# Kernel tuning notes

Measured on AMD Instinct MI355X. Metric: run time of the kernel, lower is better.

Reference implementation:

```python
import jax, jax.numpy as jnp
import numpy as np

EPS_POOL = 1e-9
NEG_INF = -1e9
TEMPERATURE = 0.07


def _l2norm(x, axis=-1, eps=1e-12):
    # matches torch F.normalize(p=2): x / max(||x||, eps)
    n = jnp.sqrt(jnp.sum(x * x, axis=axis, keepdims=True))
    return x / jnp.maximum(n, eps)


def setup_inputs() -> dict:
    key = jax.random.key(0)
    ks = jax.random.split(key, 8)
    B, Lq, Lc, D = 256, 128, 512, 384
    question_tokens = jax.random.normal(ks[0], (B, Lq, D), dtype=jnp.float32)
    chunk_tokens = jax.random.normal(ks[1], (B, Lc, D), dtype=jnp.float32)
    q_mask = jax.random.randint(ks[2], (B, Lq), 0, 2, dtype=jnp.int32)
    c_mask = jax.random.randint(ks[3], (B, Lc), 0, 2, dtype=jnp.int32)
    # ensure at least one valid token per row (avoid fully-masked rows)
    q_mask = q_mask.at[:, 0].set(1)
    c_mask = c_mask.at[:, 0].set(1)
    W1 = jax.random.normal(ks[4], (D, D), dtype=jnp.float32) * (1.0 / np.sqrt(D))
    b1 = jnp.zeros((D,), dtype=jnp.float32)
    W2 = jax.random.normal(ks[5], (D, D), dtype=jnp.float32) * (1.0 / np.sqrt(D))
    b2 = jnp.zeros((D,), dtype=jnp.float32)
    return {"question_tokens": question_tokens, "chunk_tokens": chunk_tokens,
            "q_mask": q_mask, "c_mask": c_mask,
            "W1": W1, "b1": b1, "W2": W2, "b2": b2}


def _encode(tokens, mask, W1, b1, W2, b2):
    # mean pool over valid tokens: [B,L,D] -> [B,D]
    m = mask.astype(tokens.dtype)[..., None]
    pooled = jnp.sum(tokens * m, axis=1) / jnp.maximum(jnp.sum(m, axis=1), EPS_POOL)
    h = jax.nn.relu(pooled @ W1 + b1)
    proj = h @ W2 + b2
    return _l2norm(proj, axis=1)


def _late_interaction(q_tokens, c_tokens, q_mask, c_mask):
    qn = _l2norm(q_tokens)                      # [B,Lq,D]
    cn = _l2norm(c_tokens)                      # [B,Lc,D]
    sims = jnp.einsum('bqd,bkd->bqk', qn, cn)   # [B,Lq,Lc]
    valid = q_mask[:, :, None].astype(bool) & c_mask[:, None, :].astype(bool)
    sims = jnp.where(valid, sims, NEG_INF)
    max_sim = jnp.max(sims, axis=-1)            # [B,Lq]
    max_sim = jnp.where(q_mask.astype(bool), max_sim, 0.0)
    return jnp.sum(max_sim, axis=-1)            # [B]


def reference(question_tokens, chunk_tokens, q_mask, c_mask, W1, b1, W2, b2):
    q_emb = _encode(question_tokens, q_mask, W1, b1, W2, b2)  # [B,D]
    c_emb = _encode(chunk_tokens, c_mask, W1, b1, W2, b2)     # [B,D]
    contrastive_sim = (q_emb @ c_emb.T) / TEMPERATURE         # [B,B]
    late_sim = _late_interaction(question_tokens, chunk_tokens, q_mask, c_mask)  # [B]
    return contrastive_sim, late_sim
```

## Files before the change

### kernel.cpp

```cpp
#include <hip/hip_runtime.h>
#include <hip/hip_bf16.h>
#include <stdint.h>

#define NB 256
#define LQ 128
#define LC 512
#define DIM 384
#define TCD 32
#define QP 392

typedef __attribute__((ext_vector_type(8))) short short8;
typedef __attribute__((ext_vector_type(4))) float f32x4;

__device__ __forceinline__ unsigned short f2bf(float x) {
  union { float f; uint32_t u; } c; c.f = x;
  return (unsigned short)((c.u + 0x7fffu + ((c.u >> 16) & 1u)) >> 16);
}

__global__ __launch_bounds__(512, 1)
void fused_pool_late(const float* __restrict__ qtok, const float* __restrict__ ctok,
                     const int* __restrict__ qm, const int* __restrict__ cm,
                     float* __restrict__ pooled, float* __restrict__ late) {
  __shared__ unsigned short s_q[LQ][QP];
  __shared__ unsigned short s_c[TCD][QP];
  __shared__ float s_pq[8][DIM];
  __shared__ float s_pc[8][DIM];
  __shared__ float s_cnt[2][8];
  __shared__ int   s_cval[TCD];
  __shared__ float s_wsum[8];

  const int b = blockIdx.x;
  const int tid = threadIdx.x;
  const int wave = tid >> 6;
  const int lane = tid & 63;
  const int rA = lane & 15;
  const int kof = (lane >> 4) * 8;

  const float* qb = qtok + (size_t)b * LQ * DIM;
  const float* cb = ctok + (size_t)b * LC * DIM;
  const int* qmb = qm + b * LQ;
  const int* cmb = cm + b * LC;

  float pq[6] = {0.f,0.f,0.f,0.f,0.f,0.f};
  float cq = 0.f;
  for (int r0 = 0; r0 < 16; ++r0) {
    const int r = wave * 16 + r0;
    const float* src = qb + r * DIM;
    float v[6], ss = 0.f;
#pragma unroll
    for (int j = 0; j < 6; ++j) { v[j] = src[lane + 64 * j]; ss += v[j] * v[j]; }
#pragma unroll
    for (int o = 32; o; o >>= 1) ss += __shfl_xor(ss, o);
    const float inv = 1.0f / fmaxf(sqrtf(ss), 1e-12f);
    const float fm = (float)qmb[r];
#pragma unroll
    for (int j = 0; j < 6; ++j) {
      s_q[r][lane + 64 * j] = f2bf(v[j] * inv);
      pq[j] = fmaf(v[j], fm, pq[j]);
    }
    cq += fm;
  }
#pragma unroll
  for (int j = 0; j < 6; ++j) s_pq[wave][lane + 64 * j] = pq[j];
  if (lane == 0) s_cnt[0][wave] = cq;

  float rm[4] = {-1e9f, -1e9f, -1e9f, -1e9f};
  float pc[6] = {0.f,0.f,0.f,0.f,0.f,0.f};
  float cc = 0.f;

  for (int t = 0; t < LC / TCD; ++t) {
    __syncthreads();
#pragma unroll
    for (int r0 = 0; r0 < 4; ++r0) {
      const int r = wave * 4 + r0;
      const int crow = t * TCD + r;
      const float* src = cb + crow * DIM;
      float v[6], ss = 0.f;
#pragma unroll
      for (int j = 0; j < 6; ++j) { v[j] = src[lane + 64 * j]; ss += v[j] * v[j]; }
#pragma unroll
      for (int o = 32; o; o >>= 1) ss += __shfl_xor(ss, o);
      const float inv = 1.0f / fmaxf(sqrtf(ss), 1e-12f);
      const int mk = cmb[crow];
      const float fm = (float)mk;
#pragma unroll
      for (int j = 0; j < 6; ++j) {
        s_c[r][lane + 64 * j] = f2bf(v[j] * inv);
        pc[j] = fmaf(v[j], fm, pc[j]);
      }
      cc += fm;
      if (lane == 0) s_cval[r] = mk;
    }
    __syncthreads();

    const unsigned short* ap  = &s_q[wave * 16 + rA][kof];
    const unsigned short* bp0 = &s_c[rA][kof];
    const unsigned short* bp1 = &s_c[rA + 16][kof];
    f32x4 acc0 = {0.f,0.f,0.f,0.f};
    f32x4 acc1 = {0.f,0.f,0.f,0.f};
#pragma unroll
    for (int kk = 0; kk < 12; ++kk) {
      short8 a  = *(const short8*)(ap  + kk * 32);
      short8 b0 = *(const short8*)(bp0 + kk * 32);
      short8 b1 = *(const short8*)(bp1 + kk * 32);
      acc0 = __builtin_amdgcn_mfma_f32_16x16x32_bf16(a, b0, acc0, 0, 0, 0);
      acc1 = __builtin_amdgcn_mfma_f32_16x16x32_bf16(a, b1, acc1, 0, 0, 0);
    }
    const bool v0 = s_cval[rA] != 0;
    const bool v1 = s_cval[rA + 16] != 0;
#pragma unroll
    for (int r = 0; r < 4; ++r) {
      const float a0 = v0 ? acc0[r] : -1e9f;
      const float a1 = v1 ? acc1[r] : -1e9f;
      rm[r] = fmaxf(rm[r], fmaxf(a0, a1));
    }
  }

#pragma unroll
  for (int j = 0; j < 6; ++j) s_pc[wave][lane + 64 * j] = pc[j];
  if (lane == 0) s_cnt[1][wave] = cc;

#pragma unroll
  for (int r = 0; r < 4; ++r) {
#pragma unroll
    for (int o = 1; o < 16; o <<= 1) rm[r] = fmaxf(rm[r], __shfl_xor(rm[r], o));
  }
  float ps = 0.f;
  if (rA == 0) {
    const int rowb = wave * 16 + (lane >> 4) * 4;
#pragma unroll
    for (int r = 0; r < 4; ++r) ps += qmb[rowb + r] ? rm[r] : 0.f;
  }
#pragma unroll
  for (int o = 32; o; o >>= 1) ps += __shfl_xor(ps, o);
  if (lane == 0) s_wsum[wave] = ps;
  __syncthreads();

  if (tid < DIM) {
    float sq = 0.f, sc = 0.f, nq = 0.f, nc = 0.f;
#pragma unroll
    for (int w = 0; w < 8; ++w) {
      sq += s_pq[w][tid];
      sc += s_pc[w][tid];
      nq += s_cnt[0][w];
      nc += s_cnt[1][w];
    }
    pooled[b * DIM + tid] = sq / fmaxf(nq, 1e-9f);
    pooled[(NB + b) * DIM + tid] = sc / fmaxf(nc, 1e-9f);
  }
  if (tid == 0) {
    float tot = 0.f;
#pragma unroll
    for (int w = 0; w < 8; ++w) tot += s_wsum[w];
    late[b] = tot;
  }
}

__global__ __launch_bounds__(DIM)
void mlp_kernel(const float* __restrict__ pooled,
                const float* __restrict__ W1, const float* __restrict__ b1,
                const float* __restrict__ W2, const float* __restrict__ b2,
                float* __restrict__ emb) {
  __shared__ float s_in[DIM];
  __shared__ float s_h[DIM];
  __shared__ float s_red[6];
  const int row = blockIdx.y * NB + blockIdx.x;
  const int d = threadIdx.x;
  s_in[d] = pooled[row * DIM + d];
  __syncthreads();
  float acc = b1[d];
#pragma unroll 8
  for (int k = 0; k < DIM; ++k) acc = fmaf(s_in[k], W1[k * DIM + d], acc);
  s_h[d] = fmaxf(acc, 0.f);
  __syncthreads();
  float p = b2[d];
#pragma unroll 8
  for (int k = 0; k < DIM; ++k) p = fmaf(s_h[k], W2[k * DIM + d], p);
  float ss = p * p;
#pragma unroll
  for (int o = 32; o; o >>= 1) ss += __shfl_xor(ss, o);
  if ((d & 63) == 0) s_red[d >> 6] = ss;
  __syncthreads();
  float tot = 0.f;
#pragma unroll
  for (int w = 0; w < 6; ++w) tot += s_red[w];
  emb[row * DIM + d] = p * (1.0f / fmaxf(sqrtf(tot), 1e-12f));
}

__global__ __launch_bounds__(NB)
void contrast_kernel(const float* __restrict__ emb, float* __restrict__ out0) {
  __shared__ float s_q[DIM];
  const int i = blockIdx.x;
  for (int k = threadIdx.x; k < DIM; k += NB) s_q[k] = emb[i * DIM + k];
  __syncthreads();
  const float* ce = emb + (size_t)(NB + threadIdx.x) * DIM;
  float acc = 0.f;
#pragma unroll 8
  for (int k = 0; k < DIM; ++k) acc = fmaf(s_q[k], ce[k], acc);
  out0[i * NB + threadIdx.x] = acc / 0.07f;
}

extern "C" void kernel_launch(void* const* d_in, const int* in_sizes, int n_in,
                              void* d_out, int out_size, void* d_ws, size_t ws_size,
                              hipStream_t stream) {
  const float* qtok = (const float*)d_in[0];
  const float* ctok = (const float*)d_in[1];
  const int*   qmm  = (const int*)d_in[2];
  const int*   cmm  = (const int*)d_in[3];
  const float* W1   = (const float*)d_in[4];
  const float* b1   = (const float*)d_in[5];
  const float* W2   = (const float*)d_in[6];
  const float* b2   = (const float*)d_in[7];

  float* out0 = (float*)d_out;
  float* late = out0 + NB * NB;
  float* pooled = (float*)d_ws;
  float* emb    = pooled + 2 * NB * DIM;

  hipLaunchKernelGGL(fused_pool_late, dim3(NB), dim3(512), 0, stream,
                     qtok, ctok, qmm, cmm, pooled, late);
  hipLaunchKernelGGL(mlp_kernel, dim3(NB, 2), dim3(DIM), 0, stream,
                     pooled, W1, b1, W2, b2, emb);
  hipLaunchKernelGGL(contrast_kernel, dim3(NB), dim3(NB), 0, stream, emb, out0);
}
```

Measured before the change: 134.7 us.

## Split fused pool/late kernel into normalize, pipelined maxsim, and merged MLP stages

Replaces the single 256-block fused kernel with a wide normalize+pool pass that writes bf16 normalized tokens to workspace. A separate maxsim kernel then reads them through a triple-buffered global_load_lds pipeline with swizzled LDS and register-held A fragments. A merge kernel runs the q and c MLPs together, sharing weight loads. The goal is more parallelism across CUs and overlap of loads with MFMA, at the cost of an extra bf16 round trip through HBM and a large workspace requirement. The old path is kept as a fallback when the workspace is too small.

```diff
diff --git a/kernel.cpp b/kernel.cpp
--- a/kernel.cpp
+++ b/kernel.cpp
@@ -6,21 +6,296 @@
 #define LQ 128
 #define LC 512
 #define DIM 384
+
+typedef __attribute__((ext_vector_type(8))) short short8;
+typedef __attribute__((ext_vector_type(4))) float f4;
+typedef __attribute__((ext_vector_type(2))) unsigned int u32x2;
+
+__device__ __forceinline__ unsigned int pk2bf(float a, float b) {
+  union { float f; uint32_t u; } x, y; x.f = a; y.f = b;
+  uint32_t lo = (x.u + 0x7fffu + ((x.u >> 16) & 1u)) >> 16;
+  uint32_t hi = (y.u + 0x7fffu + ((y.u >> 16) & 1u)) >> 16;
+  return lo | (hi << 16);
+}
+
+__device__ __forceinline__ void gload16(const void* g, void* l) {
+  __builtin_amdgcn_global_load_lds(
+      (const __attribute__((address_space(1))) void*)g,
+      (__attribute__((address_space(3))) void*)l, 16, 0, 0);
+}
+
+__device__ __forceinline__ void barrier_pinned() {
+  __builtin_amdgcn_sched_barrier(0);
+  __builtin_amdgcn_s_barrier();
+  __builtin_amdgcn_sched_barrier(0);
+}
+
+__device__ __forceinline__ void proc_row(const float* __restrict__ src, int mk,
+                                         unsigned short* __restrict__ dst, int lane,
+                                         f4& p0, f4& p1, float& cnt) {
+  const f4* p = (const f4*)src;
+  const f4 va = p[lane];
+  const f4 vb = p[64 + (lane & 31)];
+  float ss = va.x*va.x + va.y*va.y + va.z*va.z + va.w*va.w;
+  if (lane < 32) ss += vb.x*vb.x + vb.y*vb.y + vb.z*vb.z + vb.w*vb.w;
+#pragma unroll
+  for (int o = 32; o; o >>= 1) ss += __shfl_xor(ss, o);
+  const float inv = 1.0f / fmaxf(sqrtf(ss), 1e-12f);
+  const float fm = (float)mk;
+  p0 += va * fm;
+  if (lane < 32) p1 += vb * fm;
+  cnt += fm;
+  u32x2 w0; w0[0] = pk2bf(va.x * inv, va.y * inv); w0[1] = pk2bf(va.z * inv, va.w * inv);
+  *(u32x2*)(dst + 4 * lane) = w0;
+  if (lane < 32) {
+    u32x2 w1; w1[0] = pk2bf(vb.x * inv, vb.y * inv); w1[1] = pk2bf(vb.z * inv, vb.w * inv);
+    *(u32x2*)(dst + 256 + 4 * lane) = w1;
+  }
+}
+
+__global__ __launch_bounds__(256, 8)
+void normalize_pool(const float* __restrict__ qtok, const float* __restrict__ ctok,
+                    const int* __restrict__ qm, const int* __restrict__ cm,
+                    unsigned short* __restrict__ qn, unsigned short* __restrict__ cn,
+                    float* __restrict__ pp, float* __restrict__ nn) {
+  __shared__ float s_red[4][2][DIM];
+  __shared__ float s_cnt[4][2];
+  const int bid = blockIdx.x;
+  const int b = bid >> 3, s = bid & 7;
+  const int tid = threadIdx.x, wave = tid >> 6, lane = tid & 63;
+
+  f4 pq0 = {0,0,0,0}, pq1 = {0,0,0,0}, pc0 = {0,0,0,0}, pc1 = {0,0,0,0};
+  float cq = 0.f, cc = 0.f;
+
+#pragma unroll
+  for (int i = 0; i < 4; ++i) {
+    const int row = b * LQ + s * 16 + wave * 4 + i;
+    proc_row(qtok + (size_t)row * DIM, qm[row], qn + (size_t)row * DIM, lane, pq0, pq1, cq);
+  }
+#pragma unroll 4
+  for (int i = 0; i < 16; ++i) {
+    const int row = b * LC + s * 64 + wave * 16 + i;
+    proc_row(ctok + (size_t)row * DIM, cm[row], cn + (size_t)row * DIM, lane, pc0, pc1, cc);
+  }
+
+  *(f4*)&s_red[wave][0][4 * lane] = pq0;
+  if (lane < 32) *(f4*)&s_red[wave][0][256 + 4 * lane] = pq1;
+  *(f4*)&s_red[wave][1][4 * lane] = pc0;
+  if (lane < 32) *(f4*)&s_red[wave][1][256 + 4 * lane] = pc1;
+  if (lane == 0) { s_cnt[wave][0] = cq; s_cnt[wave][1] = cc; }
+  __syncthreads();
+
+  for (int d = tid; d < DIM; d += 256) {
+    float sq = 0.f, sc = 0.f;
+#pragma unroll
+    for (int w = 0; w < 4; ++w) { sq += s_red[w][0][d]; sc += s_red[w][1][d]; }
+    pp[(size_t)bid * 768 + d] = sq;
+    pp[(size_t)bid * 768 + DIM + d] = sc;
+  }
+  if (tid == 0) {
+    nn[bid * 2]     = s_cnt[0][0] + s_cnt[1][0] + s_cnt[2][0] + s_cnt[3][0];
+    nn[bid * 2 + 1] = s_cnt[0][1] + s_cnt[1][1] + s_cnt[2][1] + s_cnt[3][1];
+  }
+}
+
+__global__ __launch_bounds__(512, 4)
+void maxsim(const unsigned short* __restrict__ qn, const unsigned short* __restrict__ cn,
+            const int* __restrict__ cm, float* __restrict__ ws_rm) {
+  __shared__ __attribute__((aligned(128))) char ring[3][24576];
+  __shared__ int s_cm[256];
+  const int bid = blockIdx.x;
+  const int b = bid >> 1, s = bid & 1;
+  const int tid = threadIdx.x, wave = tid >> 6, lane = tid & 63;
+  const int rA = lane & 15, hi = lane >> 4;
+
+  if (tid < 256) s_cm[tid] = cm[b * LC + s * 256 + tid];
+  __syncthreads();
+
+  const char* qbase = (const char*)(qn + (size_t)b * LQ * DIM);
+  const char* cbase = (const char*)(cn + (size_t)b * LC * DIM) + (size_t)s * 256 * 768;
+
+  int goff[3];
+#pragma unroll
+  for (int j = 0; j < 3; ++j) {
+    const unsigned n = (unsigned)j * 512u + (unsigned)wave * 64u + (unsigned)lane;
+    const unsigned row = n / 48u, col = n % 48u;
+    goff[j] = (int)(row * 768u + ((col ^ (row & 7u)) << 4));
+  }
+
+#pragma unroll
+  for (int tile = 0; tile < 3; ++tile) {
+    char* dst = ring[tile] + wave * 1024;
+#pragma unroll
+    for (int j = 0; j < 3; ++j) gload16(qbase + tile * 24576 + goff[j], dst + j * 8192);
+  }
+  asm volatile("s_waitcnt vmcnt(0)" ::: "memory");
+  barrier_pinned();
+
+  short8 A[12] = {};
+  if (wave < 6) {
+    const char* bp = ring[wave >> 1];
+    const int lr = (wave & 1) * 16 + rA;
+#pragma unroll
+    for (int kk = 0; kk < 12; ++kk)
+      A[kk] = *(const short8*)(bp + lr * 768 + (((kk * 4 + hi) ^ (lr & 7)) << 4));
+    asm volatile("s_waitcnt lgkmcnt(0)" ::: "memory");
+  }
+  barrier_pinned();
+
+  {
+    char* dst = ring[0] + wave * 1024;
+#pragma unroll
+    for (int j = 0; j < 3; ++j) gload16(qbase + 3 * 24576 + goff[j], dst + j * 8192);
+  }
+  asm volatile("s_waitcnt vmcnt(0)" ::: "memory");
+  barrier_pinned();
+  if (wave >= 6) {
+    const char* bp = ring[0];
+    const int lr = (wave - 6) * 16 + rA;
+#pragma unroll
+    for (int kk = 0; kk < 12; ++kk)
+      A[kk] = *(const short8*)(bp + lr * 768 + (((kk * 4 + hi) ^ (lr & 7)) << 4));
+    asm volatile("s_waitcnt lgkmcnt(0)" ::: "memory");
+  }
+  barrier_pinned();
+
+#pragma unroll
+  for (int t0 = 0; t0 < 2; ++t0) {
+    char* dst = ring[t0 + 1] + wave * 1024;
+#pragma unroll
+    for (int j = 0; j < 3; ++j) gload16(cbase + (size_t)t0 * 24576 + goff[j], dst + j * 8192);
+  }
+
+  float rm[4] = {-1e9f, -1e9f, -1e9f, -1e9f};
+
+#pragma unroll
+  for (int t = 0; t < 8; ++t) {
+    if (t == 7) { asm volatile("s_waitcnt vmcnt(0)" ::: "memory"); }
+    else        { asm volatile("s_waitcnt vmcnt(3)" ::: "memory"); }
+    barrier_pinned();
+
+    const char* bp = ring[(t + 1) % 3];
+    f4 acc0 = {0,0,0,0}, acc1 = {0,0,0,0};
+#pragma unroll
+    for (int kk = 0; kk < 12; ++kk) {
+      const int sw = ((kk * 4 + hi) ^ (rA & 7)) << 4;
+      const short8 b0 = *(const short8*)(bp + rA * 768 + sw);
+      const short8 b1 = *(const short8*)(bp + (rA + 16) * 768 + sw);
+      acc0 = __builtin_amdgcn_mfma_f32_16x16x32_bf16(A[kk], b0, acc0, 0, 0, 0);
+      acc1 = __builtin_amdgcn_mfma_f32_16x16x32_bf16(A[kk], b1, acc1, 0, 0, 0);
+    }
+    if (t + 2 < 8) {
+      char* dst = ring[(t + 3) % 3] + wave * 1024;
+#pragma unroll
+      for (int j = 0; j < 3; ++j) gload16(cbase + (size_t)(t + 2) * 24576 + goff[j], dst + j * 8192);
+    }
+    const bool v0 = s_cm[t * 32 + rA] != 0;
+    const bool v1 = s_cm[t * 32 + rA + 16] != 0;
+#pragma unroll
+    for (int r = 0; r < 4; ++r) {
+      const float a0 = v0 ? acc0[r] : -1e9f;
+      const float a1 = v1 ? acc1[r] : -1e9f;
+      rm[r] = fmaxf(rm[r], fmaxf(a0, a1));
+    }
+  }
+
+#pragma unroll
+  for (int r = 0; r < 4; ++r) {
+#pragma unroll
+    for (int o = 1; o < 16; o <<= 1) rm[r] = fmaxf(rm[r], __shfl_xor(rm[r], o));
+  }
+  if (rA == 0) {
+#pragma unroll
+    for (int r = 0; r < 4; ++r)
+      ws_rm[(size_t)bid * LQ + wave * 16 + hi * 4 + r] = rm[r];
+  }
+}
+
+__global__ __launch_bounds__(DIM)
+void merge_mlp(const float* __restrict__ ws_rm, const float* __restrict__ pp,
+               const float* __restrict__ nn, const int* __restrict__ qm,
+               const float* __restrict__ W1, const float* __restrict__ b1,
+               const float* __restrict__ W2, const float* __restrict__ b2,
+               float* __restrict__ late, float* __restrict__ emb) {
+  __shared__ float s_q[DIM], s_c[DIM], s_hq[DIM], s_hc[DIM];
+  __shared__ float s_red[2][6], s_l[2];
+  const int b = blockIdx.x;
+  const int d = threadIdx.x;
+
+  if (d < LQ) {
+    const float m = fmaxf(ws_rm[(size_t)(2 * b) * LQ + d],
+                          ws_rm[(size_t)(2 * b + 1) * LQ + d]);
+    float ps = qm[b * LQ + d] ? m : 0.f;
+#pragma unroll
+    for (int o = 32; o; o >>= 1) ps += __shfl_xor(ps, o);
+    if ((d & 63) == 0) s_l[d >> 6] = ps;
+  }
+  float sq = 0.f, sc = 0.f, nq = 0.f, nc = 0.f;
+#pragma unroll
+  for (int s = 0; s < 8; ++s) {
+    sq += pp[(size_t)(b * 8 + s) * 768 + d];
+    sc += pp[(size_t)(b * 8 + s) * 768 + DIM + d];
+    nq += nn[(b * 8 + s) * 2];
+    nc += nn[(b * 8 + s) * 2 + 1];
+  }
+  s_q[d] = sq / fmaxf(nq, 1e-9f);
+  s_c[d] = sc / fmaxf(nc, 1e-9f);
+  __syncthreads();
+
+  float aq = b1[d], ac = b1[d];
+#pragma unroll 8
+  for (int k = 0; k < DIM; ++k) {
+    const float w = W1[k * DIM + d];
+    aq = fmaf(s_q[k], w, aq);
+    ac = fmaf(s_c[k], w, ac);
+  }
+  s_hq[d] = fmaxf(aq, 0.f);
+  s_hc[d] = fmaxf(ac, 0.f);
+  __syncthreads();
+  float pq = b2[d], pc = b2[d];
+#pragma unroll 8
+  for (int k = 0; k < DIM; ++k) {
+    const float w = W2[k * DIM + d];
+    pq = fmaf(s_hq[k], w, pq);
+    pc = fmaf(s_hc[k], w, pc);
+  }
+  float q2 = pq * pq, c2 = pc * pc;
+#pragma unroll
+  for (int o = 32; o; o >>= 1) { q2 += __shfl_xor(q2, o); c2 += __shfl_xor(c2, o); }
+  if ((d & 63) == 0) { s_red[0][d >> 6] = q2; s_red[1][d >> 6] = c2; }
+  __syncthreads();
+  float tq = 0.f, tc = 0.f;
+#pragma unroll
+  for (int w = 0; w < 6; ++w) { tq += s_red[0][w]; tc += s_red[1][w]; }
+  emb[(size_t)b * DIM + d] = pq * (1.0f / fmaxf(sqrtf(tq), 1e-12f));
+  emb[(size_t)(NB + b) * DIM + d] = pc * (1.0f / fmaxf(sqrtf(tc), 1e-12f));
+  if (d == 0) late[b] = s_l[0] + s_l[1];
+}
+
+__global__ __launch_bounds__(NB)
+void contrast_kernel(const float* __restrict__ emb, float* __restrict__ out0) {
+  __shared__ float s_q[DIM];
+  const int i = blockIdx.x;
+  for (int k = threadIdx.x; k < DIM; k += NB) s_q[k] = emb[(size_t)i * DIM + k];
+  __syncthreads();
+  const float* ce = emb + (size_t)(NB + threadIdx.x) * DIM;
+  float acc = 0.f;
+#pragma unroll 8
+  for (int k = 0; k < DIM; ++k) acc = fmaf(s_q[k], ce[k], acc);
+  out0[(size_t)i * NB + threadIdx.x] = acc / 0.07f;
+}
+
 #define TCD 32
 #define QP 392
-
-typedef __attribute__((ext_vector_type(8))) short short8;
-typedef __attribute__((ext_vector_type(4))) float f32x4;
-
 __device__ __forceinline__ unsigned short f2bf(float x) {
   union { float f; uint32_t u; } c; c.f = x;
   return (unsigned short)((c.u + 0x7fffu + ((c.u >> 16) & 1u)) >> 16);
 }
 
 __global__ __launch_bounds__(512, 1)
-void fused_pool_late(const float* __restrict__ qtok, const float* __restrict__ ctok,
-                     const int* __restrict__ qm, const int* __restrict__ cm,
-                     float* __restrict__ pooled, float* __restrict__ late) {
+void fused_v1(const float* __restrict__ qtok, const float* __restrict__ ctok,
+              const int* __restrict__ qm, const int* __restrict__ cm,
+              float* __restrict__ pooled, float* __restrict__ late) {
   __shared__ unsigned short s_q[LQ][QP];
   __shared__ unsigned short s_c[TCD][QP];
   __shared__ float s_pq[8][DIM];
@@ -96,8 +371,8 @@
     const unsigned short* ap  = &s_q[wave * 16 + rA][kof];
     const unsigned short* bp0 = &s_c[rA][kof];
     const unsigned short* bp1 = &s_c[rA + 16][kof];
-    f32x4 acc0 = {0.f,0.f,0.f,0.f};
-    f32x4 acc1 = {0.f,0.f,0.f,0.f};
+    f4 acc0 = {0.f,0.f,0.f,0.f};
+    f4 acc1 = {0.f,0.f,0.f,0.f};
 #pragma unroll
     for (int kk = 0; kk < 12; ++kk) {
       short8 a  = *(const short8*)(ap  + kk * 32);
@@ -157,16 +432,16 @@
 }
 
 __global__ __launch_bounds__(DIM)
-void mlp_kernel(const float* __restrict__ pooled,
-                const float* __restrict__ W1, const float* __restrict__ b1,
-                const float* __restrict__ W2, const float* __restrict__ b2,
-                float* __restrict__ emb) {
+void mlp_v1(const float* __restrict__ pooled,
+            const float* __restrict__ W1, const float* __restrict__ b1,
+            const float* __restrict__ W2, const float* __restrict__ b2,
+            float* __restrict__ emb) {
   __shared__ float s_in[DIM];
   __shared__ float s_h[DIM];
   __shared__ float s_red[6];
   const int row = blockIdx.y * NB + blockIdx.x;
   const int d = threadIdx.x;
-  s_in[d] = pooled[row * DIM + d];
+  s_in[d] = pooled[(size_t)row * DIM + d];
   __syncthreads();
   float acc = b1[d];
 #pragma unroll 8
@@ -184,20 +459,7 @@
   float tot = 0.f;
 #pragma unroll
   for (int w = 0; w < 6; ++w) tot += s_red[w];
-  emb[row * DIM + d] = p * (1.0f / fmaxf(sqrtf(tot), 1e-12f));
-}
-
-__global__ __launch_bounds__(NB)
-void contrast_kernel(const float* __restrict__ emb, float* __restrict__ out0) {
-  __shared__ float s_q[DIM];
-  const int i = blockIdx.x;
-  for (int k = threadIdx.x; k < DIM; k += NB) s_q[k] = emb[i * DIM + k];
-  __syncthreads();
-  const float* ce = emb + (size_t)(NB + threadIdx.x) * DIM;
-  float acc = 0.f;
-#pragma unroll 8
-  for (int k = 0; k < DIM; ++k) acc = fmaf(s_q[k], ce[k], acc);
-  out0[i * NB + threadIdx.x] = acc / 0.07f;
+  emb[(size_t)row * DIM + d] = p * (1.0f / fmaxf(sqrtf(tot), 1e-12f));
 }
 
 extern "C" void kernel_launch(void* const* d_in, const int* in_sizes, int n_in,
@@ -214,12 +476,36 @@
 
   float* out0 = (float*)d_out;
   float* late = out0 + NB * NB;
-  float* pooled = (float*)d_ws;
-  float* emb    = pooled + 2 * NB * DIM;
-
-  hipLaunchKernelGGL(fused_pool_late, dim3(NB), dim3(512), 0, stream,
-                     qtok, ctok, qmm, cmm, pooled, late);
-  hipLaunchKernelGGL(mlp_kernel, dim3(NB, 2), dim3(DIM), 0, stream,
-                     pooled, W1, b1, W2, b2, emb);
-  hipLaunchKernelGGL(contrast_kernel, dim3(NB), dim3(NB), 0, stream, emb, out0);
-}
+
+  const size_t PP_N   = (size_t)2048 * 768;
+  const size_t NN_N   = 4096;
+  const size_t RM_N   = (size_t)512 * LQ;
+  const size_t EMB_N  = (size_t)2 * NB * DIM;
+  const size_t QN_N   = (size_t)NB * LQ * DIM;
+  const size_t CN_N   = (size_t)NB * LC * DIM;
+  const size_t NEED   = (PP_N + NN_N + RM_N + EMB_N) * 4 + (QN_N + CN_N) * 2;
+
+  if (ws_size >= NEED) {
+    float* pp  = (float*)d_ws;
+    float* nn  = pp + PP_N;
+    float* rm  = nn + NN_N;
+    float* emb = rm + RM_N;
+    unsigned short* qn = (unsigned short*)(emb + EMB_N);
+    unsigned short* cn = qn + QN_N;
+
+    hipLaunchKernelGGL(normalize_pool, dim3(2048), dim3(256), 0, stream,
+                       qtok, ctok, qmm, cmm, qn, cn, pp, nn);
+    hipLaunchKernelGGL(maxsim, dim3(512), dim3(512), 0, stream, qn, cn, cmm, rm);
+    hipLaunchKernelGGL(merge_mlp, dim3(NB), dim3(DIM), 0, stream,
+                       rm, pp, nn, qmm, W1, b1, W2, b2, late, emb);
+    hipLaunchKernelGGL(contrast_kernel, dim3(NB), dim3(NB), 0, stream, emb, out0);
+  } else {
+    float* pooled = (float*)d_ws;
+    float* emb    = pooled + 2 * NB * DIM;
+    hipLaunchKernelGGL(fused_v1, dim3(NB), dim3(512), 0, stream,
+                       qtok, ctok, qmm, cmm, pooled, late);
+    hipLaunchKernelGGL(mlp_v1, dim3(NB, 2), dim3(DIM), 0, stream,
+                       pooled, W1, b1, W2, b2, emb);
+    hipLaunchKernelGGL(contrast_kernel, dim3(NB), dim3(NB), 0, stream, emb, out0);
+  }
+}
```

Result: slower. 209.6 us (+55.6%).

## Pipeline token loads with double-buffered LDS and keep Q fragments in registers

Applied to the files above, without the earlier changes.

Rewrites the fused pooling/late-interaction kernel as a 20-stage software pipeline: global float4 loads for stage t+2 are issued while stage t is converted to bf16 in a double-buffered LDS tile, with explicit vmcnt waits. The L2 normalization is moved out of the bf16 data and applied as per-row inverse-norm scaling after the MFMA. Each wave holds its Q fragments in registers, LDS shrinks so two blocks can fit per CU, and masks are staged in shared memory. This targets HBM load latency and LDS pressure, at the cost of much more complex scheduling and a small numeric change from scaling after the bf16 product.

```diff
diff --git a/kernel.cpp b/kernel.cpp
--- a/kernel.cpp
+++ b/kernel.cpp
@@ -6,119 +6,164 @@
 #define LQ 128
 #define LC 512
 #define DIM 384
-#define TCD 32
-#define QP 392
+#define CBP 392
+#define NST 20
 
 typedef __attribute__((ext_vector_type(8))) short short8;
-typedef __attribute__((ext_vector_type(4))) float f32x4;
-
-__device__ __forceinline__ unsigned short f2bf(float x) {
-  union { float f; uint32_t u; } c; c.f = x;
-  return (unsigned short)((c.u + 0x7fffu + ((c.u >> 16) & 1u)) >> 16);
-}
-
-__global__ __launch_bounds__(512, 1)
-void fused_pool_late(const float* __restrict__ qtok, const float* __restrict__ ctok,
-                     const int* __restrict__ qm, const int* __restrict__ cm,
-                     float* __restrict__ pooled, float* __restrict__ late) {
-  __shared__ unsigned short s_q[LQ][QP];
-  __shared__ unsigned short s_c[TCD][QP];
-  __shared__ float s_pq[8][DIM];
-  __shared__ float s_pc[8][DIM];
-  __shared__ float s_cnt[2][8];
-  __shared__ int   s_cval[TCD];
+typedef __attribute__((ext_vector_type(4))) float f4;
+typedef __attribute__((ext_vector_type(2))) unsigned int u32x2;
+
+__device__ __forceinline__ unsigned int pk2bf(float a, float b) {
+  union { float f; uint32_t u; } x, y; x.f = a; y.f = b;
+  uint32_t lo = (x.u + 0x7fffu + ((x.u >> 16) & 1u)) >> 16;
+  uint32_t hi = (y.u + 0x7fffu + ((y.u >> 16) & 1u)) >> 16;
+  return lo | (hi << 16);
+}
+
+__global__ __launch_bounds__(512, 2)
+void fused2(const float* __restrict__ qtok, const float* __restrict__ ctok,
+            const int* __restrict__ qm, const int* __restrict__ cm,
+            float* __restrict__ pooled, float* __restrict__ late) {
+  __shared__ unsigned short s_cb[2][32][CBP];
+  __shared__ float s_qi[LQ];
+  __shared__ float s_ci[2][32];
+  __shared__ int s_qm[LQ];
+  __shared__ int s_cm[LC];
+  __shared__ float s_cnt[16];
   __shared__ float s_wsum[8];
 
-  const int b = blockIdx.x;
-  const int tid = threadIdx.x;
-  const int wave = tid >> 6;
-  const int lane = tid & 63;
-  const int rA = lane & 15;
-  const int kof = (lane >> 4) * 8;
+  const int b = blockIdx.x, tid = threadIdx.x;
+  const int wave = tid >> 6, lane = tid & 63;
+  const int rA = lane & 15, hi = lane >> 4;
+  const bool hiHalf = lane >= 32;
+  const int l31 = lane & 31;
 
   const float* qb = qtok + (size_t)b * LQ * DIM;
   const float* cb = ctok + (size_t)b * LC * DIM;
-  const int* qmb = qm + b * LQ;
-  const int* cmb = cm + b * LC;
-
-  float pq[6] = {0.f,0.f,0.f,0.f,0.f,0.f};
-  float cq = 0.f;
-  for (int r0 = 0; r0 < 16; ++r0) {
-    const int r = wave * 16 + r0;
-    const float* src = qb + r * DIM;
-    float v[6], ss = 0.f;
-#pragma unroll
-    for (int j = 0; j < 6; ++j) { v[j] = src[lane + 64 * j]; ss += v[j] * v[j]; }
-#pragma unroll
-    for (int o = 32; o; o >>= 1) ss += __shfl_xor(ss, o);
-    const float inv = 1.0f / fmaxf(sqrtf(ss), 1e-12f);
-    const float fm = (float)qmb[r];
-#pragma unroll
-    for (int j = 0; j < 6; ++j) {
-      s_q[r][lane + 64 * j] = f2bf(v[j] * inv);
-      pq[j] = fmaf(v[j], fm, pq[j]);
-    }
-    cq += fm;
-  }
-#pragma unroll
-  for (int j = 0; j < 6; ++j) s_pq[wave][lane + 64 * j] = pq[j];
-  if (lane == 0) s_cnt[0][wave] = cq;
-
+
+  s_cm[tid] = cm[b * LC + tid];
+  if (tid < LQ) s_qm[tid] = qm[b * LQ + tid];
+  __syncthreads();
+
+  f4 v0[4], h0[2], v1[4], h1[2];
+  f4 pqA = {0,0,0,0}, pqB = {0,0,0,0}, pcA = {0,0,0,0}, pcB = {0,0,0,0};
+  float cq = 0.f, cc = 0.f;
   float rm[4] = {-1e9f, -1e9f, -1e9f, -1e9f};
-  float pc[6] = {0.f,0.f,0.f,0.f,0.f,0.f};
-  float cc = 0.f;
-
-  for (int t = 0; t < LC / TCD; ++t) {
-    __syncthreads();
-#pragma unroll
-    for (int r0 = 0; r0 < 4; ++r0) {
-      const int r = wave * 4 + r0;
-      const int crow = t * TCD + r;
-      const float* src = cb + crow * DIM;
-      float v[6], ss = 0.f;
-#pragma unroll
-      for (int j = 0; j < 6; ++j) { v[j] = src[lane + 64 * j]; ss += v[j] * v[j]; }
-#pragma unroll
-      for (int o = 32; o; o >>= 1) ss += __shfl_xor(ss, o);
-      const float inv = 1.0f / fmaxf(sqrtf(ss), 1e-12f);
-      const int mk = cmb[crow];
-      const float fm = (float)mk;
-#pragma unroll
-      for (int j = 0; j < 6; ++j) {
-        s_c[r][lane + 64 * j] = f2bf(v[j] * inv);
-        pc[j] = fmaf(v[j], fm, pc[j]);
-      }
-      cc += fm;
-      if (lane == 0) s_cval[r] = mk;
-    }
-    __syncthreads();
-
-    const unsigned short* ap  = &s_q[wave * 16 + rA][kof];
-    const unsigned short* bp0 = &s_c[rA][kof];
-    const unsigned short* bp1 = &s_c[rA + 16][kof];
-    f32x4 acc0 = {0.f,0.f,0.f,0.f};
-    f32x4 acc1 = {0.f,0.f,0.f,0.f};
-#pragma unroll
-    for (int kk = 0; kk < 12; ++kk) {
-      short8 a  = *(const short8*)(ap  + kk * 32);
-      short8 b0 = *(const short8*)(bp0 + kk * 32);
-      short8 b1 = *(const short8*)(bp1 + kk * 32);
-      acc0 = __builtin_amdgcn_mfma_f32_16x16x32_bf16(a, b0, acc0, 0, 0, 0);
-      acc1 = __builtin_amdgcn_mfma_f32_16x16x32_bf16(a, b1, acc1, 0, 0, 0);
-    }
-    const bool v0 = s_cval[rA] != 0;
-    const bool v1 = s_cval[rA + 16] != 0;
-#pragma unroll
-    for (int r = 0; r < 4; ++r) {
-      const float a0 = v0 ? acc0[r] : -1e9f;
-      const float a1 = v1 ? acc1[r] : -1e9f;
-      rm[r] = fmaxf(rm[r], fmaxf(a0, a1));
-    }
-  }
-
-#pragma unroll
-  for (int j = 0; j < 6; ++j) s_pc[wave][lane + 64 * j] = pc[j];
-  if (lane == 0) s_cnt[1][wave] = cc;
+  short8 A[12] = {};
+
+#define TBASE(t) (((t) < 4) ? (qb + (size_t)(t) * 32 * DIM) \
+                            : (cb + (size_t)((t) - 4) * 32 * DIM))
+
+#define ISSUE(V, H, base_) do {                                              \
+    const float* bb_ = (base_);                                              \
+    _Pragma("unroll")                                                        \
+    for (int i_ = 0; i_ < 4; ++i_)                                           \
+      V[i_] = *((const f4*)(bb_ + (size_t)(wave * 4 + i_) * DIM) + lane);    \
+    _Pragma("unroll")                                                        \
+    for (int j_ = 0; j_ < 2; ++j_)                                           \
+      H[j_] = *((const f4*)(bb_ + (size_t)(wave * 4 + 2 * j_ +               \
+                (hiHalf ? 1 : 0)) * DIM) + 64 + l31);                        \
+  } while (0)
+
+#define STAGE(T, V, H, BUF) do {                                             \
+    const int t_ = (T);                                                      \
+    if (t_ == NST - 1) { asm volatile("s_waitcnt vmcnt(0)" ::: "memory"); }  \
+    else               { asm volatile("s_waitcnt vmcnt(6)" ::: "memory"); }  \
+    __builtin_amdgcn_sched_barrier(0);                                       \
+    const bool isq_ = t_ < 4;                                                \
+    const int* mk_ = isq_ ? (s_qm + t_ * 32) : (s_cm + (t_ - 4) * 32);       \
+    float ss_[4];                                                            \
+    _Pragma("unroll")                                                        \
+    for (int i_ = 0; i_ < 4; ++i_) {                                         \
+      const int lr_ = wave * 4 + i_;                                         \
+      u32x2 w_; w_[0] = pk2bf(V[i_].x, V[i_].y); w_[1] = pk2bf(V[i_].z, V[i_].w); \
+      *(u32x2*)&s_cb[BUF][lr_][4 * lane] = w_;                               \
+      ss_[i_] = V[i_].x * V[i_].x + V[i_].y * V[i_].y                        \
+              + V[i_].z * V[i_].z + V[i_].w * V[i_].w;                       \
+    }                                                                        \
+    _Pragma("unroll")                                                        \
+    for (int j_ = 0; j_ < 2; ++j_) {                                         \
+      const int lr_ = wave * 4 + 2 * j_ + (hiHalf ? 1 : 0);                  \
+      u32x2 w_; w_[0] = pk2bf(H[j_].x, H[j_].y); w_[1] = pk2bf(H[j_].z, H[j_].w); \
+      *(u32x2*)&s_cb[BUF][lr_][256 + 4 * l31] = w_;                          \
+      const float td_ = H[j_].x * H[j_].x + H[j_].y * H[j_].y               \
+                      + H[j_].z * H[j_].z + H[j_].w * H[j_].w;              \
+      if (hiHalf) ss_[2 * j_ + 1] += td_; else ss_[2 * j_] += td_;           \
+    }                                                                        \
+    _Pragma("unroll")                                                        \
+    for (int o_ = 32; o_; o_ >>= 1) {                                        \
+      _Pragma("unroll")                                                      \
+      for (int i_ = 0; i_ < 4; ++i_) ss_[i_] += __shfl_xor(ss_[i_], o_);     \
+    }                                                                        \
+    float fm_[4];                                                            \
+    _Pragma("unroll")                                                        \
+    for (int i_ = 0; i_ < 4; ++i_) fm_[i_] = (float)mk_[wave * 4 + i_];      \
+    if (isq_) {                                                              \
+      _Pragma("unroll")                                                      \
+      for (int i_ = 0; i_ < 4; ++i_) { pqA += V[i_] * fm_[i_]; cq += fm_[i_]; } \
+      _Pragma("unroll")                                                      \
+      for (int j_ = 0; j_ < 2; ++j_)                                         \
+        pqB += H[j_] * (hiHalf ? fm_[2 * j_ + 1] : fm_[2 * j_]);             \
+      if (lane == 0) {                                                       \
+        _Pragma("unroll")                                                    \
+        for (int i_ = 0; i_ < 4; ++i_)                                       \
+          s_qi[t_ * 32 + wave * 4 + i_] = 1.0f / fmaxf(sqrtf(ss_[i_]), 1e-12f); \
+      }                                                                      \
+    } else {                                                                 \
+      _Pragma("unroll")                                                      \
+      for (int i_ = 0; i_ < 4; ++i_) { pcA += V[i_] * fm_[i_]; cc += fm_[i_]; } \
+      _Pragma("unroll")                                                      \
+      for (int j_ = 0; j_ < 2; ++j_)                                         \
+        pcB += H[j_] * (hiHalf ? fm_[2 * j_ + 1] : fm_[2 * j_]);             \
+      if (lane == 0) {                                                       \
+        _Pragma("unroll")                                                    \
+        for (int i_ = 0; i_ < 4; ++i_)                                       \
+          s_ci[BUF][wave * 4 + i_] = 1.0f / fmaxf(sqrtf(ss_[i_]), 1e-12f);   \
+      }                                                                      \
+    }                                                                        \
+    if (t_ + 2 < NST) { ISSUE(V, H, TBASE(t_ + 2)); }                        \
+    asm volatile("s_waitcnt lgkmcnt(0)" ::: "memory");                       \
+    __builtin_amdgcn_s_barrier();                                            \
+    __builtin_amdgcn_sched_barrier(0);                                       \
+    if (isq_) {                                                              \
+      if ((wave >> 1) == t_) {                                               \
+        const int lb_ = (wave & 1) * 16 + rA;                                \
+        _Pragma("unroll")                                                    \
+        for (int kk_ = 0; kk_ < 12; ++kk_)                                   \
+          A[kk_] = *(const short8*)&s_cb[BUF][lb_][kk_ * 32 + hi * 8];       \
+        asm volatile("s_waitcnt lgkmcnt(0)" ::: "memory");                   \
+        __builtin_amdgcn_sched_barrier(0);                                   \
+      }                                                                      \
+    } else {                                                                 \
+      f4 a0_ = {0,0,0,0}, a1_ = {0,0,0,0};                                   \
+      _Pragma("unroll")                                                      \
+      for (int kk_ = 0; kk_ < 12; ++kk_) {                                   \
+        const short8 b0_ = *(const short8*)&s_cb[BUF][rA][kk_ * 32 + hi * 8];     \
+        const short8 b1_ = *(const short8*)&s_cb[BUF][rA + 16][kk_ * 32 + hi * 8];\
+        a0_ = __builtin_amdgcn_mfma_f32_16x16x32_bf16(A[kk_], b0_, a0_, 0, 0, 0); \
+        a1_ = __builtin_amdgcn_mfma_f32_16x16x32_bf16(A[kk_], b1_, a1_, 0, 0, 0); \
+      }                                                                      \
+      const int tb_ = (t_ - 4) * 32;                                         \
+      const bool m0_ = s_cm[tb_ + rA] != 0;                                  \
+      const bool m1_ = s_cm[tb_ + rA + 16] != 0;                             \
+      const float ci0_ = s_ci[BUF][rA], ci1_ = s_ci[BUF][rA + 16];           \
+      _Pragma("unroll")                                                      \
+      for (int r_ = 0; r_ < 4; ++r_) {                                       \
+        const float qi_ = s_qi[wave * 16 + hi * 4 + r_];                     \
+        const float x0_ = m0_ ? a0_[r_] * (qi_ * ci0_) : -1e9f;              \
+        const float x1_ = m1_ ? a1_[r_] * (qi_ * ci1_) : -1e9f;              \
+        rm[r_] = fmaxf(rm[r_], fmaxf(x0_, x1_));                             \
+      }                                                                      \
+    }                                                                        \
+  } while (0)
+
+  ISSUE(v0, h0, TBASE(0));
+  ISSUE(v1, h1, TBASE(1));
+
+  for (int t = 0; t < NST; t += 2) {
+    STAGE(t, v0, h0, 0);
+    STAGE(t + 1, v1, h1, 1);
+  }
 
 #pragma unroll
   for (int r = 0; r < 4; ++r) {
@@ -127,24 +172,41 @@
   }
   float ps = 0.f;
   if (rA == 0) {
-    const int rowb = wave * 16 + (lane >> 4) * 4;
-#pragma unroll
-    for (int r = 0; r < 4; ++r) ps += qmb[rowb + r] ? rm[r] : 0.f;
+    const int rowb = wave * 16 + hi * 4;
+#pragma unroll
+    for (int r = 0; r < 4; ++r) ps += s_qm[rowb + r] ? rm[r] : 0.f;
   }
 #pragma unroll
   for (int o = 32; o; o >>= 1) ps += __shfl_xor(ps, o);
   if (lane == 0) s_wsum[wave] = ps;
+
+  __syncthreads();
+
+  float* red = (float*)&s_cb[0][0][0];
+  *(f4*)&red[(wave * 2 + 0) * 512 + 4 * lane] = pqA;
+  *(f4*)&red[(wave * 2 + 0) * 512 + 256 + (hiHalf ? 128 : 0) + 4 * l31] = pqB;
+  *(f4*)&red[(wave * 2 + 1) * 512 + 4 * lane] = pcA;
+  *(f4*)&red[(wave * 2 + 1) * 512 + 256 + (hiHalf ? 128 : 0) + 4 * l31] = pcB;
+  if (lane == 0) { s_cnt[wave] = cq; s_cnt[8 + wave] = cc; }
   __syncthreads();
 
   if (tid < DIM) {
     float sq = 0.f, sc = 0.f, nq = 0.f, nc = 0.f;
-#pragma unroll
-    for (int w = 0; w < 8; ++w) {
-      sq += s_pq[w][tid];
-      sc += s_pc[w][tid];
-      nq += s_cnt[0][w];
-      nc += s_cnt[1][w];
+    if (tid < 256) {
+#pragma unroll
+      for (int w = 0; w < 8; ++w) {
+        sq += red[(w * 2 + 0) * 512 + tid];
+        sc += red[(w * 2 + 1) * 512 + tid];
+      }
+    } else {
+#pragma unroll
+      for (int w = 0; w < 8; ++w) {
+        sq += red[(w * 2 + 0) * 512 + tid] + red[(w * 2 + 0) * 512 + tid + 128];
+        sc += red[(w * 2 + 1) * 512 + tid] + red[(w * 2 + 1) * 512 + tid + 128];
+      }
     }
+#pragma unroll
+    for (int w = 0; w < 8; ++w) { nq += s_cnt[w]; nc += s_cnt[8 + w]; }
     pooled[b * DIM + tid] = sq / fmaxf(nq, 1e-9f);
     pooled[(NB + b) * DIM + tid] = sc / fmaxf(nc, 1e-9f);
   }
@@ -157,16 +219,16 @@
 }
 
 __global__ __launch_bounds__(DIM)
-void mlp_kernel(const float* __restrict__ pooled,
-                const float* __restrict__ W1, const float* __restrict__ b1,
-                const float* __restrict__ W2, const float* __restrict__ b2,
-                float* __restrict__ emb) {
+void mlp_v1(const float* __restrict__ pooled,
+            const float* __restrict__ W1, const float* __restrict__ b1,
+            const float* __restrict__ W2, const float* __restrict__ b2,
+            float* __restrict__ emb) {
   __shared__ float s_in[DIM];
   __shared__ float s_h[DIM];
   __shared__ float s_red[6];
   const int row = blockIdx.y * NB + blockIdx.x;
   const int d = threadIdx.x;
-  s_in[d] = pooled[row * DIM + d];
+  s_in[d] = pooled[(size_t)row * DIM + d];
   __syncthreads();
   float acc = b1[d];
 #pragma unroll 8
@@ -184,20 +246,20 @@
   float tot = 0.f;
 #pragma unroll
   for (int w = 0; w < 6; ++w) tot += s_red[w];
-  emb[row * DIM + d] = p * (1.0f / fmaxf(sqrtf(tot), 1e-12f));
+  emb[(size_t)row * DIM + d] = p * (1.0f / fmaxf(sqrtf(tot), 1e-12f));
 }
 
 __global__ __launch_bounds__(NB)
 void contrast_kernel(const float* __restrict__ emb, float* __restrict__ out0) {
   __shared__ float s_q[DIM];
   const int i = blockIdx.x;
-  for (int k = threadIdx.x; k < DIM; k += NB) s_q[k] = emb[i * DIM + k];
+  for (int k = threadIdx.x; k < DIM; k += NB) s_q[k] = emb[(size_t)i * DIM + k];
   __syncthreads();
   const float* ce = emb + (size_t)(NB + threadIdx.x) * DIM;
   float acc = 0.f;
 #pragma unroll 8
   for (int k = 0; k < DIM; ++k) acc = fmaf(s_q[k], ce[k], acc);
-  out0[i * NB + threadIdx.x] = acc / 0.07f;
+  out0[(size_t)i * NB + threadIdx.x] = acc / 0.07f;
 }
 
 extern "C" void kernel_launch(void* const* d_in, const int* in_sizes, int n_in,
@@ -217,9 +279,9 @@
   float* pooled = (float*)d_ws;
   float* emb    = pooled + 2 * NB * DIM;
 
-  hipLaunchKernelGGL(fused_pool_late, dim3(NB), dim3(512), 0, stream,
+  hipLaunchKernelGGL(fused2, dim3(NB), dim3(512), 0, stream,
                      qtok, ctok, qmm, cmm, pooled, late);
-  hipLaunchKernelGGL(mlp_kernel, dim3(NB, 2), dim3(DIM), 0, stream,
+  hipLaunchKernelGGL(mlp_v1, dim3(NB, 2), dim3(DIM), 0, stream,
                      pooled, W1, b1, W2, b2, emb);
   hipLaunchKernelGGL(contrast_kernel, dim3(NB), dim3(NB), 0, stream, emb, out0);
 }
```

Result: faster. 108.5 us (-19.5%).
